# Kernel optimization log

Measured on AMD Instinct MI355X. Metric: run time of the kernel, lower is better.

The kernel has to match this reference:

```python
import jax, jax.numpy as jnp
import numpy as np

N_NODES = 100000
N_EDGES = 3200000
D_IN = 128
D_HID = 128
N_CLASSES = 40


def setup_inputs() -> dict:
    key = jax.random.key(0)
    ks = jax.random.split(key, 8)
    x = jax.random.normal(ks[0], (N_NODES, D_IN), dtype=jnp.float32)
    edge_index = jax.random.randint(ks[1], (2, N_EDGES), 0, N_NODES, dtype=jnp.int64)
    s1 = 1.0 / np.sqrt(D_IN)
    s2 = 1.0 / np.sqrt(D_HID)
    W1 = jax.random.normal(ks[2], (D_IN, D_HID), dtype=jnp.float32) * s1
    b1 = jnp.zeros((D_HID,), dtype=jnp.float32)
    W2 = jax.random.normal(ks[3], (D_HID, D_HID), dtype=jnp.float32) * s2
    b2 = jnp.zeros((D_HID,), dtype=jnp.float32)
    Wl = jax.random.normal(ks[4], (D_HID, N_CLASSES), dtype=jnp.float32) * s2
    bl = jnp.zeros((N_CLASSES,), dtype=jnp.float32)
    return {"x": x, "edge_index": edge_index, "W1": W1, "b1": b1,
            "W2": W2, "b2": b2, "Wl": Wl, "bl": bl}


def _gcn_conv(x, W, b, src, dst, inv_sqrt_deg, n_nodes):
    # h = X @ W  (linear transform first: cheaper when out_dim <= in_dim)
    h = x @ W  # [N, d_out]
    # symmetric normalization: norm_e = deg(src)^-1/2 * deg(dst)^-1/2
    norm = inv_sqrt_deg[src] * inv_sqrt_deg[dst]  # [E]
    msg = h[src] * norm[:, None]                  # gather + scale  [E, d_out]
    out = jax.ops.segment_sum(msg, dst, num_segments=n_nodes)  # scatter-add
    return out + b


def reference(x, edge_index, W1, b1, W2, b2, Wl, bl):
    n = x.shape[0]
    # GCNConv adds self-loops before normalization (PyG default)
    loops = jnp.arange(n, dtype=edge_index.dtype)
    src = jnp.concatenate([edge_index[0], loops])
    dst = jnp.concatenate([edge_index[1], loops])
    deg = jax.ops.segment_sum(jnp.ones_like(dst, dtype=x.dtype), dst, num_segments=n)
    inv_sqrt_deg = jnp.where(deg > 0, jax.lax.rsqrt(deg), 0.0)

    h = _gcn_conv(x, W1, b1, src, dst, inv_sqrt_deg, n)
    h = jax.nn.relu(h)
    h = _gcn_conv(h, W2, b2, src, dst, inv_sqrt_deg, n)
    h = jax.nn.relu(h)
    return h @ Wl + bl
```

## Files before the change

### kernel.cpp

```cpp
#include <hip/hip_runtime.h>
#include <hip/hip_bf16.h>

typedef _Float16 f16;
typedef _Float16 f16x8 __attribute__((ext_vector_type(8)));

#define D 128
#define N_CLS 40
#define BN 128
#define NBMAX 1024

__global__ __launch_bounds__(256) void k_hist(const int* __restrict__ dst,
                                              int* __restrict__ bcnt, int e) {
  __shared__ int lh[NBMAX];
  for (int j = threadIdx.x; j < NBMAX; j += 256) lh[j] = 0;
  __syncthreads();
  int stride = gridDim.x * blockDim.x;
  for (int q = blockIdx.x * blockDim.x + threadIdx.x; q < e; q += stride)
    atomicAdd(&lh[dst[q] >> 7], 1);
  __syncthreads();
  for (int j = threadIdx.x; j < NBMAX; j += 256)
    if (lh[j]) atomicAdd(&bcnt[j], lh[j]);
}

__global__ __launch_bounds__(1024) void k_bscan(const int* __restrict__ bcnt,
                                                int* __restrict__ bbase,
                                                int* __restrict__ bcur) {
  __shared__ int sums[NBMAX];
  int t = threadIdx.x;
  int c = bcnt[t];
  sums[t] = c;
  __syncthreads();
  for (int off = 1; off < NBMAX; off <<= 1) {
    int a = (t >= off) ? sums[t - off] : 0;
    __syncthreads();
    sums[t] += a;
    __syncthreads();
  }
  bbase[t] = sums[t] - c;
  bcur[t] = sums[t] - c;
}

__global__ __launch_bounds__(256) void k_place(const int* __restrict__ src,
                                               const int* __restrict__ dst,
                                               int* __restrict__ bcur,
                                               unsigned int* __restrict__ binned,
                                               int e, int nwg) {
  __shared__ int lh[NBMAX];
  __shared__ int lofs[NBMAX];
  __shared__ int lcur[NBMAX];
  int chunk = (e + nwg - 1) / nwg;
  int lo = blockIdx.x * chunk;
  int hi = min(e, lo + chunk);
  int t = threadIdx.x;
  for (int j = t; j < NBMAX; j += 256) { lh[j] = 0; lcur[j] = 0; }
  __syncthreads();
  for (int q = lo + t; q < hi; q += 256) atomicAdd(&lh[dst[q] >> 7], 1);
  __syncthreads();
  for (int j = t; j < NBMAX; j += 256) {
    int c = lh[j];
    lofs[j] = c ? atomicAdd(&bcur[j], c) : 0;
  }
  __syncthreads();
  for (int q = lo + t; q < hi; q += 256) {
    int d = dst[q];
    int b = d >> 7;
    int r = atomicAdd(&lcur[b], 1);
    binned[lofs[b] + r] = ((unsigned int)(d & 127) << 17) | (unsigned int)src[q];
  }
}

__global__ __launch_bounds__(256) void k_csr(const unsigned int* __restrict__ binned,
                                             const int* __restrict__ bbase,
                                             int* __restrict__ csr,
                                             int* __restrict__ deg,
                                             float* __restrict__ isd,
                                             int* __restrict__ row_start, int n) {
  int b = blockIdx.x;
  int lo = bbase[b], hi = bbase[b + 1];
  __shared__ int h[BN];
  __shared__ int sc[BN];
  __shared__ int cur[BN];
  int t = threadIdx.x;
  if (t < BN) h[t] = 0;
  __syncthreads();
  for (int q = lo + t; q < hi; q += 256) atomicAdd(&h[binned[q] >> 17], 1);
  __syncthreads();
  if (t < BN) sc[t] = h[t];
  __syncthreads();
  for (int off = 1; off < BN; off <<= 1) {
    int a = 0;
    if (t < BN && t >= off) a = sc[t - off];
    __syncthreads();
    if (t < BN) sc[t] += a;
    __syncthreads();
  }
  if (t < BN) {
    int excl = sc[t] - h[t];
    cur[t] = lo + excl;
    int i = b * BN + t;
    if (i < n) {
      deg[i] = h[t];
      isd[i] = rsqrtf((float)(h[t] + 1));
      row_start[i] = lo + excl;
    }
  }
  __syncthreads();
  for (int q = lo + t; q < hi; q += 256) {
    unsigned int u = binned[q];
    int p = atomicAdd(&cur[u >> 17], 1);
    csr[p] = (int)(u & 0x1FFFF);
  }
}

template <bool HALF_IN>
__global__ __launch_bounds__(256) void k_gemm_t(const void* __restrict__ Xv,
                                                const float* __restrict__ W,
                                                const float* __restrict__ isd,
                                                f16* __restrict__ HS, int n) {
  __shared__ float Xt[64][D + 4];
  __shared__ float Wb[32][D + 4];
  int t = threadIdx.x;
  int r0 = blockIdx.x * 64;
  if (!HALF_IN) {
    const float* X = (const float*)Xv;
    for (int q = t; q < 64 * 32; q += 256) {
      int row = q >> 5, cb = (q & 31) << 2;
      float4 v = {0.f, 0.f, 0.f, 0.f};
      if (r0 + row < n) v = *(const float4*)(X + (size_t)(r0 + row) * D + cb);
      *(float4*)&Xt[row][cb] = v;
    }
  } else {
    const f16* X = (const f16*)Xv;
    for (int q = t; q < 64 * 16; q += 256) {
      int row = q >> 4, cb = (q & 15) << 3;
      f16x8 v = 0;
      if (r0 + row < n) v = *(const f16x8*)(X + (size_t)(r0 + row) * D + cb);
      float* xp = &Xt[row][cb];
#pragma unroll
      for (int j = 0; j < 8; ++j) xp[j] = (float)v[j];
    }
  }
  int tr = ((t >> 4) & 15) << 2;
  int tc = (t & 15) << 3;
  float acc[4][8];
#pragma unroll
  for (int i = 0; i < 4; ++i)
#pragma unroll
    for (int j = 0; j < 8; ++j) acc[i][j] = 0.f;

  for (int hh = 0; hh < 4; ++hh) {
    __syncthreads();
    for (int q = t; q < 32 * 32; q += 256) {
      int row = q >> 5, cb = (q & 31) << 2;
      *(float4*)&Wb[row][cb] = *(const float4*)(W + (size_t)(hh * 32 + row) * D + cb);
    }
    __syncthreads();
#pragma unroll 4
    for (int k = 0; k < 32; ++k) {
      float4 u0 = *(const float4*)&Wb[k][tc];
      float4 u1 = *(const float4*)&Wb[k][tc + 4];
      float bv[8] = {u0.x, u0.y, u0.z, u0.w, u1.x, u1.y, u1.z, u1.w};
      int kk = hh * 32 + k;
#pragma unroll
      for (int i = 0; i < 4; ++i) {
        float a = Xt[tr + i][kk];
#pragma unroll
        for (int j = 0; j < 8; ++j) acc[i][j] += a * bv[j];
      }
    }
  }
#pragma unroll
  for (int i = 0; i < 4; ++i) {
    int row = r0 + tr + i;
    if (row < n) {
      float s = isd[row];
      f16x8 ov;
#pragma unroll
      for (int j = 0; j < 8; ++j) ov[j] = (f16)(s * acc[i][j]);
      *(f16x8*)(HS + (size_t)row * D + tc) = ov;
    }
  }
}

__device__ inline void gather8(const f16* __restrict__ HS,
                               const int* __restrict__ csr,
                               int start, int c, int lane, float acc[8]) {
  const int g = lane >> 4;
  const char* base = (const char*)HS + ((lane & 15) << 4);
  const int* __restrict__ cp = csr + start;
#pragma unroll
  for (int j = 0; j < 8; ++j) acc[j] = 0.f;

  for (int u = 0; u < c; u += 32) {
    int eg = u + g;
    int ec = c - 1;
    int sA[8];
#pragma unroll
    for (int k = 0; k < 8; ++k) {
      int ee = eg + (k << 2);
      sA[k] = cp[ee < ec ? ee : ec];
    }
    f16x8 v[8];
#pragma unroll
    for (int k = 0; k < 8; ++k) {
      v[k] = (f16x8)0;
      if (eg + (k << 2) < c)
        v[k] = *(const f16x8*)(base + ((size_t)(unsigned)sA[k] << 8));
    }
    f16x8 A = (v[0] + v[1]) + (v[2] + v[3]);
    f16x8 B = (v[4] + v[5]) + (v[6] + v[7]);
#pragma unroll
    for (int j = 0; j < 8; ++j) acc[j] += (float)A[j] + (float)B[j];
  }
#pragma unroll
  for (int j = 0; j < 8; ++j) {
    float t = acc[j];
    t += __shfl_xor(t, 16);
    t += __shfl_xor(t, 32);
    acc[j] = t;
  }
}

__global__ __launch_bounds__(256) void k_agg1(const f16* __restrict__ HS,
                                              const int* __restrict__ csr,
                                              const int* __restrict__ row_start,
                                              const int* __restrict__ deg,
                                              const float* __restrict__ isd,
                                              const float* __restrict__ bias,
                                              f16* __restrict__ G, int n) {
  int i = (blockIdx.x << 2) + (threadIdx.x >> 6);
  if (i >= n) return;
  int lane = threadIdx.x & 63;
  int l = lane & 15;
  f16x8 sv = *(const f16x8*)(HS + (size_t)i * D + l * 8);
  float di = isd[i];
  float4 bb0 = *(const float4*)(bias + l * 8);
  float4 bb1 = *(const float4*)(bias + l * 8 + 4);
  float acc[8];
  gather8(HS, csr, row_start[i], deg[i], lane, acc);
  float bv[8] = {bb0.x, bb0.y, bb0.z, bb0.w, bb1.x, bb1.y, bb1.z, bb1.w};
  f16x8 ov;
#pragma unroll
  for (int j = 0; j < 8; ++j) {
    float v = di * (acc[j] + (float)sv[j]) + bv[j];
    v = v > 0.f ? v : 0.f;
    ov[j] = (f16)v;
  }
  if ((lane >> 4) == 0) *(f16x8*)(G + (size_t)i * D + l * 8) = ov;
}

__global__ __launch_bounds__(256) void k_agg_cls(const f16* __restrict__ HS,
                                                 const int* __restrict__ csr,
                                                 const int* __restrict__ row_start,
                                                 const int* __restrict__ deg,
                                                 const float* __restrict__ isd,
                                                 const float* __restrict__ b2,
                                                 const float* __restrict__ Wl,
                                                 const float* __restrict__ bl,
                                                 float* __restrict__ out, int n) {
  int wv = threadIdx.x >> 6;
  int ir = (blockIdx.x << 2) + wv;
  int i = ir < n ? ir : n - 1;
  int lane = threadIdx.x & 63;
  int l = lane & 15;
  f16x8 sv = *(const f16x8*)(HS + (size_t)i * D + l * 8);
  float di = isd[i];
  float4 bb0 = *(const float4*)(b2 + l * 8);
  float4 bb1 = *(const float4*)(b2 + l * 8 + 4);
  float acc[8];
  gather8(HS, csr, row_start[i], deg[i], lane, acc);
  float bv[8] = {bb0.x, bb0.y, bb0.z, bb0.w, bb1.x, bb1.y, bb1.z, bb1.w};
  __shared__ float tt[4][D];
#pragma unroll
  for (int j = 0; j < 8; ++j) {
    float v = di * (acc[j] + (float)sv[j]) + bv[j];
    bv[j] = v > 0.f ? v : 0.f;
  }
  if ((lane >> 4) == 0) {
    *(float4*)&tt[wv][l * 8] = make_float4(bv[0], bv[1], bv[2], bv[3]);
    *(float4*)&tt[wv][l * 8 + 4] = make_float4(bv[4], bv[5], bv[6], bv[7]);
  }
  __syncthreads();
  if (ir < n && lane < N_CLS) {
    float o = bl[lane];
#pragma unroll 4
    for (int k = 0; k < D; k += 4) {
      float4 t4 = *(const float4*)&tt[wv][k];
      o += t4.x * Wl[(size_t)(k + 0) * N_CLS + lane];
      o += t4.y * Wl[(size_t)(k + 1) * N_CLS + lane];
      o += t4.z * Wl[(size_t)(k + 2) * N_CLS + lane];
      o += t4.w * Wl[(size_t)(k + 3) * N_CLS + lane];
    }
    out[(size_t)ir * N_CLS + lane] = o;
  }
}

extern "C" void kernel_launch(void* const* d_in, const int* in_sizes, int n_in,
                              void* d_out, int out_size, void* d_ws, size_t ws_size,
                              hipStream_t stream) {
  const float* x  = (const float*)d_in[0];
  const int*   ei = (const int*)d_in[1];
  const float* W1 = (const float*)d_in[2];
  const float* b1 = (const float*)d_in[3];
  const float* W2 = (const float*)d_in[4];
  const float* b2 = (const float*)d_in[5];
  const float* Wl = (const float*)d_in[6];
  const float* bl = (const float*)d_in[7];
  float* out = (float*)d_out;

  const int n = in_sizes[0] / D;
  const int e = in_sizes[1] / 2;
  const int* src = ei;
  const int* dst = ei + e;
  const int nb = (n + BN - 1) / BN;

  char* ws = (char*)d_ws;
  size_t off = 0;
  auto alloc = [&](size_t bytes) -> void* {
    void* p = ws + off;
    off += (bytes + 255) & ~(size_t)255;
    return p;
  };
  int*   bcnt      = (int*)alloc(NBMAX * 4);
  int*   bbase     = (int*)alloc(NBMAX * 4);
  int*   bcur      = (int*)alloc(NBMAX * 4);
  int*   deg       = (int*)alloc((size_t)n * 4);
  int*   row_start = (int*)alloc((size_t)n * 4);
  float* isd       = (float*)alloc((size_t)n * 4);
  int*   csr       = (int*)alloc((size_t)e * 4);
  f16*   hA        = (f16*)alloc((size_t)n * D * 2);
  f16*   hB        = (f16*)alloc((size_t)n * D * 2);
  unsigned int* binned = (unsigned int*)hA;

  hipMemsetAsync(bcnt, 0, NBMAX * 4, stream);

  const int nwg_place = 512;
  k_hist<<<1024, 256, 0, stream>>>(dst, bcnt, e);
  k_bscan<<<1, 1024, 0, stream>>>(bcnt, bbase, bcur);
  k_place<<<nwg_place, 256, 0, stream>>>(src, dst, bcur, binned, e, nwg_place);
  k_csr<<<nb, 256, 0, stream>>>(binned, bbase, csr, deg, isd, row_start, n);

  int gblocks = (n + 63) / 64;
  int ablocks = (n + 3) / 4;
  k_gemm_t<false><<<gblocks, 256, 0, stream>>>(x, W1, isd, hA, n);
  k_agg1<<<ablocks, 256, 0, stream>>>(hA, csr, row_start, deg, isd, b1, hB, n);
  k_gemm_t<true><<<gblocks, 256, 0, stream>>>(hB, W2, isd, hA, n);
  k_agg_cls<<<ablocks, 256, 0, stream>>>(hA, csr, row_start, deg, isd, b2, Wl, bl, out, n);
}
```

Measured before the change: 569.2 us.

## Slice feature matrix into 16-column planes for cache-local sparse gather

Stores the hidden feature matrices in a column-sliced layout of 8 planes, each holding 16 columns for every node. Aggregation blocks are assigned one slice at a time, so each gather pass reads from a 3.2 MB plane that can stay cache-resident instead of the whole 25 MB matrix. The gather now accumulates in f16 with prefetched indices, and the classifier is split into its own kernel. The costs are 8x more index reads and launches, f16 accumulation precision risk, and an extra kernel with an intermediate round trip.

```diff
diff --git a/kernel.cpp b/kernel.cpp
--- a/kernel.cpp
+++ b/kernel.cpp
@@ -8,6 +8,7 @@
 #define N_CLS 40
 #define BN 128
 #define NBMAX 1024
+
 
 __global__ __launch_bounds__(256) void k_hist(const int* __restrict__ dst,
                                               int* __restrict__ bcnt, int e) {
@@ -119,6 +120,7 @@
                                                 f16* __restrict__ HS, int n) {
   __shared__ float Xt[64][D + 4];
   __shared__ float Wb[32][D + 4];
+  const size_t ss = (size_t)n * 16;
   int t = threadIdx.x;
   int r0 = blockIdx.x * 64;
   if (!HALF_IN) {
@@ -134,7 +136,9 @@
     for (int q = t; q < 64 * 16; q += 256) {
       int row = q >> 4, cb = (q & 15) << 3;
       f16x8 v = 0;
-      if (r0 + row < n) v = *(const f16x8*)(X + (size_t)(r0 + row) * D + cb);
+      if (r0 + row < n)
+        v = *(const f16x8*)(X + (size_t)(cb >> 4) * ss +
+                            (size_t)(r0 + row) * 16 + (cb & 15));
       float* xp = &Xt[row][cb];
 #pragma unroll
       for (int j = 0; j < 8; ++j) xp[j] = (float)v[j];
@@ -177,108 +181,90 @@
       f16x8 ov;
 #pragma unroll
       for (int j = 0; j < 8; ++j) ov[j] = (f16)(s * acc[i][j]);
-      *(f16x8*)(HS + (size_t)row * D + tc) = ov;
-    }
-  }
-}
-
-__device__ inline void gather8(const f16* __restrict__ HS,
-                               const int* __restrict__ csr,
-                               int start, int c, int lane, float acc[8]) {
-  const int g = lane >> 4;
-  const char* base = (const char*)HS + ((lane & 15) << 4);
-  const int* __restrict__ cp = csr + start;
-#pragma unroll
-  for (int j = 0; j < 8; ++j) acc[j] = 0.f;
-
-  for (int u = 0; u < c; u += 32) {
-    int eg = u + g;
-    int ec = c - 1;
-    int sA[8];
-#pragma unroll
-    for (int k = 0; k < 8; ++k) {
-      int ee = eg + (k << 2);
-      sA[k] = cp[ee < ec ? ee : ec];
-    }
-    f16x8 v[8];
-#pragma unroll
-    for (int k = 0; k < 8; ++k) {
-      v[k] = (f16x8)0;
-      if (eg + (k << 2) < c)
-        v[k] = *(const f16x8*)(base + ((size_t)(unsigned)sA[k] << 8));
-    }
-    f16x8 A = (v[0] + v[1]) + (v[2] + v[3]);
-    f16x8 B = (v[4] + v[5]) + (v[6] + v[7]);
-#pragma unroll
-    for (int j = 0; j < 8; ++j) acc[j] += (float)A[j] + (float)B[j];
-  }
-#pragma unroll
-  for (int j = 0; j < 8; ++j) {
-    float t = acc[j];
-    t += __shfl_xor(t, 16);
-    t += __shfl_xor(t, 32);
-    acc[j] = t;
-  }
-}
-
-__global__ __launch_bounds__(256) void k_agg1(const f16* __restrict__ HS,
+      *(f16x8*)(HS + (size_t)(tc >> 4) * ss + (size_t)row * 16 + (tc & 15)) = ov;
+    }
+  }
+}
+
+__device__ inline f16x8 shfl_xor_f16x8(f16x8 v, int m) {
+  union { f16x8 h; int i[4]; } u;
+  u.h = v;
+#pragma unroll
+  for (int k = 0; k < 4; ++k) u.i[k] = __shfl_xor(u.i[k], m);
+  return u.h;
+}
+
+__global__ __launch_bounds__(256) void k_aggs(const f16* __restrict__ HS,
                                               const int* __restrict__ csr,
                                               const int* __restrict__ row_start,
                                               const int* __restrict__ deg,
                                               const float* __restrict__ isd,
                                               const float* __restrict__ bias,
                                               f16* __restrict__ G, int n) {
-  int i = (blockIdx.x << 2) + (threadIdx.x >> 6);
-  if (i >= n) return;
-  int lane = threadIdx.x & 63;
-  int l = lane & 15;
-  f16x8 sv = *(const f16x8*)(HS + (size_t)i * D + l * 8);
+  const size_t ss = (size_t)n * 16;
+  int t = threadIdx.x;
+  int wave = t >> 6, lane = t & 63;
+  int g = lane >> 4, r = lane & 15;
+  int s = blockIdx.x & 7;
+  int i0 = ((blockIdx.x >> 3) << 4) + (wave << 2) + g;
+  bool ok = i0 < n;
+  int i = ok ? i0 : n - 1;
+  int hf = r & 1, er = r >> 1;
+  int dg = deg[i];
+  const int* cp = csr + row_start[i];
+  const f16* sb = HS + (size_t)s * ss + (size_t)hf * 8;
+  f16x8 a0 = (f16x8)0, a1 = (f16x8)0;
+  if (dg > 0) {
+    int dgm = dg - 1;
+    int iA = cp[min(er, dgm)];
+    int iB = cp[min(er + 8, dgm)];
+    for (int u = 0; u < dg; u += 16) {
+      int cA = iA, cB = iB;
+      iA = cp[min(u + 16 + er, dgm)];
+      iB = cp[min(u + 24 + er, dgm)];
+      if (u + er < dg)
+        a0 += *(const f16x8*)(sb + ((size_t)(unsigned)cA << 4));
+      if (u + 8 + er < dg)
+        a1 += *(const f16x8*)(sb + ((size_t)(unsigned)cB << 4));
+    }
+  }
+  f16x8 tv = a0 + a1;
+  tv += shfl_xor_f16x8(tv, 2);
+  tv += shfl_xor_f16x8(tv, 4);
+  tv += shfl_xor_f16x8(tv, 8);
+  f16x8 sv = *(const f16x8*)(HS + (size_t)s * ss + (size_t)i * 16 + hf * 8);
   float di = isd[i];
-  float4 bb0 = *(const float4*)(bias + l * 8);
-  float4 bb1 = *(const float4*)(bias + l * 8 + 4);
-  float acc[8];
-  gather8(HS, csr, row_start[i], deg[i], lane, acc);
-  float bv[8] = {bb0.x, bb0.y, bb0.z, bb0.w, bb1.x, bb1.y, bb1.z, bb1.w};
+  const float* bp = bias + s * 16 + hf * 8;
+  float4 b0 = *(const float4*)bp;
+  float4 b1 = *(const float4*)(bp + 4);
+  float bv[8] = {b0.x, b0.y, b0.z, b0.w, b1.x, b1.y, b1.z, b1.w};
   f16x8 ov;
 #pragma unroll
   for (int j = 0; j < 8; ++j) {
-    float v = di * (acc[j] + (float)sv[j]) + bv[j];
+    float v = di * ((float)tv[j] + (float)sv[j]) + bv[j];
     v = v > 0.f ? v : 0.f;
     ov[j] = (f16)v;
   }
-  if ((lane >> 4) == 0) *(f16x8*)(G + (size_t)i * D + l * 8) = ov;
-}
-
-__global__ __launch_bounds__(256) void k_agg_cls(const f16* __restrict__ HS,
-                                                 const int* __restrict__ csr,
-                                                 const int* __restrict__ row_start,
-                                                 const int* __restrict__ deg,
-                                                 const float* __restrict__ isd,
-                                                 const float* __restrict__ b2,
-                                                 const float* __restrict__ Wl,
-                                                 const float* __restrict__ bl,
-                                                 float* __restrict__ out, int n) {
+  if (ok && r < 2)
+    *(f16x8*)(G + (size_t)s * ss + (size_t)i * 16 + hf * 8) = ov;
+}
+
+__global__ __launch_bounds__(256) void k_cls(const f16* __restrict__ H,
+                                             const float* __restrict__ Wl,
+                                             const float* __restrict__ bl,
+                                             float* __restrict__ out, int n) {
+  const size_t ss = (size_t)n * 16;
   int wv = threadIdx.x >> 6;
   int ir = (blockIdx.x << 2) + wv;
   int i = ir < n ? ir : n - 1;
   int lane = threadIdx.x & 63;
-  int l = lane & 15;
-  f16x8 sv = *(const f16x8*)(HS + (size_t)i * D + l * 8);
-  float di = isd[i];
-  float4 bb0 = *(const float4*)(b2 + l * 8);
-  float4 bb1 = *(const float4*)(b2 + l * 8 + 4);
-  float acc[8];
-  gather8(HS, csr, row_start[i], deg[i], lane, acc);
-  float bv[8] = {bb0.x, bb0.y, bb0.z, bb0.w, bb1.x, bb1.y, bb1.z, bb1.w};
   __shared__ float tt[4][D];
-#pragma unroll
-  for (int j = 0; j < 8; ++j) {
-    float v = di * (acc[j] + (float)sv[j]) + bv[j];
-    bv[j] = v > 0.f ? v : 0.f;
-  }
-  if ((lane >> 4) == 0) {
-    *(float4*)&tt[wv][l * 8] = make_float4(bv[0], bv[1], bv[2], bv[3]);
-    *(float4*)&tt[wv][l * 8 + 4] = make_float4(bv[4], bv[5], bv[6], bv[7]);
+  if (lane < 16) {
+    int s = lane >> 1, hf = lane & 1;
+    f16x8 v = *(const f16x8*)(H + (size_t)s * ss + (size_t)i * 16 + hf * 8);
+    float* dp = &tt[wv][s * 16 + hf * 8];
+#pragma unroll
+    for (int j = 0; j < 8; ++j) dp[j] = (float)v[j];
   }
   __syncthreads();
   if (ir < n && lane < N_CLS) {
@@ -286,10 +272,10 @@
 #pragma unroll 4
     for (int k = 0; k < D; k += 4) {
       float4 t4 = *(const float4*)&tt[wv][k];
-      o += t4.x * Wl[(size_t)(k + 0) * N_CLS + lane];
-      o += t4.y * Wl[(size_t)(k + 1) * N_CLS + lane];
-      o += t4.z * Wl[(size_t)(k + 2) * N_CLS + lane];
-      o += t4.w * Wl[(size_t)(k + 3) * N_CLS + lane];
+      o += t4.x * Wl[(k + 0) * N_CLS + lane];
+      o += t4.y * Wl[(k + 1) * N_CLS + lane];
+      o += t4.z * Wl[(k + 2) * N_CLS + lane];
+      o += t4.w * Wl[(k + 3) * N_CLS + lane];
     }
     out[(size_t)ir * N_CLS + lane] = o;
   }
@@ -341,9 +327,10 @@
   k_csr<<<nb, 256, 0, stream>>>(binned, bbase, csr, deg, isd, row_start, n);
 
   int gblocks = (n + 63) / 64;
-  int ablocks = (n + 3) / 4;
+  int ablocks = ((n + 15) / 16) * 8;
   k_gemm_t<false><<<gblocks, 256, 0, stream>>>(x, W1, isd, hA, n);
-  k_agg1<<<ablocks, 256, 0, stream>>>(hA, csr, row_start, deg, isd, b1, hB, n);
+  k_aggs<<<ablocks, 256, 0, stream>>>(hA, csr, row_start, deg, isd, b1, hB, n);
   k_gemm_t<true><<<gblocks, 256, 0, stream>>>(hB, W2, isd, hA, n);
-  k_agg_cls<<<ablocks, 256, 0, stream>>>(hA, csr, row_start, deg, isd, b2, Wl, bl, out, n);
-}
+  k_aggs<<<ablocks, 256, 0, stream>>>(hA, csr, row_start, deg, isd, b2, hB, n);
+  k_cls<<<(n + 3) / 4, 256, 0, stream>>>(hB, Wl, bl, out, n);
+}
```

Measured after the change: 679.9 us. 19.5% more time.
